# Optimization experiments

Hardware: AMD Instinct MI355X
Metric: run time of the kernel (lower is better)

Reference implementation:

```python
import jax, jax.numpy as jnp
import numpy as np

BN_EPS = 1e-5


def _posit_intervals():
    # Replicates conditions_l1 / conditions_g1 interval tables (128 steps each).
    l1, g1 = [], []
    for e in range(16):
        for j in range(8):
            if j == 0:
                l1.append((0.0, 1.0625 / 2**16, 1.0 / 2**16))
            else:
                lo = (1.0625 + 0.125 * (j - 1)) / 2 ** (16 - e)
                hi = (1.0625 + 0.125 * j) / 2 ** (16 - e)
                l1.append((lo, hi, 0.5 * (lo + hi)))
            lo = (1.0625 + 0.125 * (j - 1)) * 2 ** e
            hi = (1.0625 + 0.125 * j) * 2 ** e
            g1.append((lo, hi, 0.5 * (lo + hi)))  # note: j==8 branch in torch code is dead
    return l1, g1

_L1, _G1 = _posit_intervals()


def posit_quantize(x):
    # Faithful emulation of the 128 sequential torch.where passes.
    ax = jnp.abs(x)          # conditions are fixed from the ORIGINAL tensor
    neg = x < 0
    y = x
    for (lo1, hi1, m1), (log_, hig, mg) in zip(_L1, _G1):
        c1 = jnp.logical_and(ax > lo1, ax < hi1)
        cg = jnp.logical_and(ax > log_, ax < hig)
        v1 = jnp.where(neg, -m1, m1).astype(x.dtype)
        vg = jnp.where(neg, -mg, mg).astype(x.dtype)
        # |y| < 1 gate uses the CURRENT tensor, as in the torch loop
        y = jnp.where(jnp.abs(y) < 1, jnp.where(c1, v1, y), jnp.where(cg, vg, y))
    return y


def conv1x1(x, w, b):
    # x: [N,C,D,H,W], w: [O,C] (kernel_size=1), b: [O]
    return jnp.einsum('ncdhw,oc->nodhw', x, w) + b[None, :, None, None, None]


def batchnorm(x, gamma, beta, mean, var):
    inv = gamma / jnp.sqrt(var + BN_EPS)
    return x * inv[None, :, None, None, None] + (beta - mean * inv)[None, :, None, None, None]


def setup_inputs() -> dict:
    key = jax.random.key(0)
    ks = jax.random.split(key, 12)
    C = 256
    x = jax.random.normal(ks[0], (8, C, 16, 32, 32), dtype=jnp.float32)
    w1 = jax.random.normal(ks[1], (C, C), dtype=jnp.float32) * 0.05
    b1 = jax.random.normal(ks[2], (C,), dtype=jnp.float32) * 0.05
    w2 = jax.random.normal(ks[3], (C, C), dtype=jnp.float32) * 0.05
    b2 = jax.random.normal(ks[4], (C,), dtype=jnp.float32) * 0.05
    g1 = jax.random.uniform(ks[5], (C,)) + 0.5
    be1 = jax.random.normal(ks[6], (C,)) * 0.1
    m1 = jax.random.normal(ks[7], (C,)) * 0.1
    v1 = jax.random.uniform(ks[8], (C,)) + 0.5
    g2 = jax.random.uniform(ks[9], (C,)) + 0.5
    be2 = jax.random.normal(ks[10], (C,)) * 0.1
    m2 = jax.random.normal(ks[11], (C,)) * 0.1
    v2 = jax.random.uniform(jax.random.fold_in(key, 99), (C,)) + 0.5
    return {"x": x, "w1": w1, "b1": b1, "g1": g1, "be1": be1, "m1": m1, "v1": v1,
            "w2": w2, "b2": b2, "g2": g2, "be2": be2, "m2": m2, "v2": v2}


def reference(x, w1, b1, g1, be1, m1, v1, w2, b2, g2, be2, m2, v2):
    residual = x
    out = conv1x1(posit_quantize(x), posit_quantize(w1), b1)
    out = jax.nn.relu(batchnorm(out, g1, be1, m1, v1))
    out = conv1x1(posit_quantize(out), posit_quantize(w2), b2)
    out = batchnorm(out, g2, be2, m2, v2)
    return jax.nn.relu(out + residual)
```

## Files before the change

### kernel.cpp

```cpp
#include <hip/hip_runtime.h>

typedef __attribute__((ext_vector_type(8))) short short8;
typedef __attribute__((ext_vector_type(4))) short s4v;
typedef __attribute__((ext_vector_type(4))) float floatx4;

#define SPOS 16384

__device__ __forceinline__ unsigned short f2bf(float f) {
    unsigned u = __float_as_uint(f);
    u += 0x7fffu + ((u >> 16) & 1u);
    return (unsigned short)(u >> 16);
}

__device__ __forceinline__ float posit_q(float x) {
    unsigned xu  = __float_as_uint(x);
    unsigned sgn = xu & 0x80000000u;
    unsigned au  = xu & 0x7fffffffu;
    unsigned m   = au & 0x007fffffu;
    unsigned r   = (au + 0x00080000u) & 0xfff00000u;
    bool bdry = (m & 0x000fffffu) == 0x00080000u;
    unsigned res;
    if (au >= 0x3f800000u) {
        res = r;
        if (m > 0x00700000u && m < 0x00780000u && au < 0x47700000u)
            res = (au & 0xff800000u) + 0x00800000u;
        if ((bdry && m != 0x00780000u) || au >= 0x47780000u)
            res = au;
    } else {
        res = (m <= 0x00080000u || m >= 0x00780000u || bdry) ? au : r;
        if (au < 0x37880000u) res = au ? 0x37800000u : 0u;
    }
    return __uint_as_float(sgn | res);
}

__global__ __launch_bounds__(256) void prep_kernel(
    const float* __restrict__ w1, const float* __restrict__ w2,
    const float* __restrict__ b1, const float* __restrict__ g1,
    const float* __restrict__ be1, const float* __restrict__ m1,
    const float* __restrict__ v1,
    const float* __restrict__ b2, const float* __restrict__ g2,
    const float* __restrict__ be2, const float* __restrict__ m2,
    const float* __restrict__ v2,
    unsigned short* __restrict__ w1q, unsigned short* __restrict__ w2q,
    float* __restrict__ cst)
{
    int i = blockIdx.x * 256 + threadIdx.x;
    if (i < 65536) {
        w1q[i] = f2bf(posit_q(w1[i]));
        w2q[i] = f2bf(posit_q(w2[i]));
        if (i < 256) {
            float inv1 = g1[i] / sqrtf(v1[i] + 1e-5f);
            cst[i]       = inv1;
            cst[256 + i] = fmaf(b1[i], inv1, be1[i] - m1[i] * inv1);
            float inv2 = g2[i] / sqrtf(v2[i] + 1e-5f);
            cst[512 + i] = inv2;
            cst[768 + i] = fmaf(b2[i], inv2, be2[i] - m2[i] * inv2);
        }
    }
}

__device__ __forceinline__ int qidx(int p, int cb) {
    return p * 256 + ((cb ^ (p & 31)) << 3);
}

__global__ __launch_bounds__(256, 3) void fused_kernel(
    const float* __restrict__ x,
    const unsigned short* __restrict__ w1q,
    const unsigned short* __restrict__ w2q,
    const float* __restrict__ cst,
    float* __restrict__ out)
{
    __shared__ alignas(16) unsigned short q[64 * 256];
    __shared__ alignas(16) float xs[64 * 64];

    const int b  = blockIdx.x;
    const int n  = b >> 8;
    const int s0 = (b & 255) << 6;
    const float* xb = x   + (size_t)n * (256 * SPOS) + s0;
    float*       ob = out + (size_t)n * (256 * SPOS) + s0;

    const int t    = threadIdx.x;
    const int lane = t & 63;
    const int w    = t >> 6;
    const int quad = lane >> 4;
    const int l15  = lane & 15;

    {
        const int g   = t & 15;
        const int ca  = t >> 4;
        for (int qt = 0; qt < 4; ++qt) {
            #pragma unroll
            for (int r = 0; r < 4; ++r) {
                const int cl = r * 16 + ca;
                const float4 v = *(const float4*)&xb[(size_t)(qt * 64 + cl) * SPOS + 4 * g];
                *(float4*)&xs[cl * 64 + 4 * g] = v;
            }
            __syncthreads();
            {
                const int p  = lane;
                const int c0 = w * 16;
                short8 pk0, pk1;
                #pragma unroll
                for (int j = 0; j < 8; ++j) {
                    pk0[j] = (short)f2bf(posit_q(xs[(c0 + j) * 64 + p]));
                    pk1[j] = (short)f2bf(posit_q(xs[(c0 + 8 + j) * 64 + p]));
                }
                const int cb0 = qt * 8 + w * 2;
                *(short8*)&q[qidx(p, cb0)]     = pk0;
                *(short8*)&q[qidx(p, cb0 + 1)] = pk1;
            }
            __syncthreads();
        }
    }

    const int mbase = w * 64;
    floatx4 acc[4][4];
    #pragma unroll
    for (int i = 0; i < 4; ++i)
        #pragma unroll
        for (int jj = 0; jj < 4; ++jj)
            acc[i][jj] = (floatx4)0.0f;

    #pragma unroll
    for (int kk = 0; kk < 256; kk += 32) {
        short8 af[4], bf[4];
        #pragma unroll
        for (int i = 0; i < 4; ++i)
            af[i] = *(const short8*)&w1q[(size_t)(mbase + 16 * i + l15) * 256 + kk + quad * 8];
        #pragma unroll
        for (int jj = 0; jj < 4; ++jj)
            bf[jj] = *(const short8*)&q[qidx(16 * jj + l15, (kk >> 3) + quad)];
        #pragma unroll
        for (int i = 0; i < 4; ++i)
            #pragma unroll
            for (int jj = 0; jj < 4; ++jj)
                acc[i][jj] = __builtin_amdgcn_mfma_f32_16x16x32_bf16(af[i], bf[jj], acc[i][jj], 0, 0, 0);
    }
    __syncthreads();

    {
        const float* sc1 = cst;
        const float* bi1 = cst + 256;
        #pragma unroll
        for (int i = 0; i < 4; ++i) {
            const int m0 = mbase + 16 * i + quad * 4;
            float sc[4], bi[4];
            #pragma unroll
            for (int r = 0; r < 4; ++r) { sc[r] = sc1[m0 + r]; bi[r] = bi1[m0 + r]; }
            #pragma unroll
            for (int jj = 0; jj < 4; ++jj) {
                const int p = 16 * jj + l15;
                s4v h;
                #pragma unroll
                for (int r = 0; r < 4; ++r) {
                    float z = fmaf(acc[i][jj][r], sc[r], bi[r]);
                    z = fmaxf(z, 0.0f);
                    h[r] = (short)f2bf(posit_q(z));
                }
                *(s4v*)&q[qidx(p, m0 >> 3) + (m0 & 7)] = h;
            }
        }
    }
    __syncthreads();

    #pragma unroll
    for (int i = 0; i < 4; ++i)
        #pragma unroll
        for (int jj = 0; jj < 4; ++jj)
            acc[i][jj] = (floatx4)0.0f;

    #pragma unroll
    for (int kk = 0; kk < 256; kk += 32) {
        short8 af[4], bf[4];
        #pragma unroll
        for (int i = 0; i < 4; ++i)
            af[i] = *(const short8*)&w2q[(size_t)(mbase + 16 * i + l15) * 256 + kk + quad * 8];
        #pragma unroll
        for (int jj = 0; jj < 4; ++jj)
            bf[jj] = *(const short8*)&q[qidx(16 * jj + l15, (kk >> 3) + quad)];
        #pragma unroll
        for (int i = 0; i < 4; ++i)
            #pragma unroll
            for (int jj = 0; jj < 4; ++jj)
                acc[i][jj] = __builtin_amdgcn_mfma_f32_16x16x32_bf16(af[i], bf[jj], acc[i][jj], 0, 0, 0);
    }

    {
        const float* sc2 = cst + 512;
        const float* bi2 = cst + 768;
        #pragma unroll
        for (int i = 0; i < 4; ++i) {
            const int m0 = mbase + 16 * i + quad * 4;
            float sc[4], bi[4];
            #pragma unroll
            for (int r = 0; r < 4; ++r) { sc[r] = sc2[m0 + r]; bi[r] = bi2[m0 + r]; }
            #pragma unroll
            for (int jj = 0; jj < 4; ++jj) {
                const int p = 16 * jj + l15;
                #pragma unroll
                for (int r = 0; r < 4; ++r) {
                    const size_t off = (size_t)(m0 + r) * SPOS + p;
                    float v = fmaf(acc[i][jj][r], sc[r], bi[r]);
                    v += xb[off];
                    ob[off] = fmaxf(v, 0.0f);
                }
            }
        }
    }
}

extern "C" void kernel_launch(void* const* d_in, const int* in_sizes, int n_in,
                              void* d_out, int out_size, void* d_ws, size_t ws_size,
                              hipStream_t stream) {
    const float* x   = (const float*)d_in[0];
    const float* w1  = (const float*)d_in[1];
    const float* b1  = (const float*)d_in[2];
    const float* g1  = (const float*)d_in[3];
    const float* be1 = (const float*)d_in[4];
    const float* m1  = (const float*)d_in[5];
    const float* v1  = (const float*)d_in[6];
    const float* w2  = (const float*)d_in[7];
    const float* b2  = (const float*)d_in[8];
    const float* g2  = (const float*)d_in[9];
    const float* be2 = (const float*)d_in[10];
    const float* m2  = (const float*)d_in[11];
    const float* v2  = (const float*)d_in[12];

    unsigned short* w1q = (unsigned short*)d_ws;
    unsigned short* w2q = w1q + 65536;
    float* cst = (float*)(w2q + 65536);

    prep_kernel<<<256, 256, 0, stream>>>(w1, w2, b1, g1, be1, m1, v1,
                                         b2, g2, be2, m2, v2, w1q, w2q, cst);
    fused_kernel<<<2048, 256, 0, stream>>>(x, w1q, w2q, cst, (float*)d_out);
}
```

Baseline: 397.8 us.

## Per-wave x staging with swizzled transpose, drop block barriers, raise occupancy

The input-staging phase changes from four block-wide tiles, each with two __syncthreads, to per-wavefront 8-channel slices in a private 2KB LDS region. Each wave loads, XOR-swizzles, quantizes and packs its own 64 channels, and a single barrier follows. The smaller LDS footprint and launch bounds raised from 3 to 4 are meant to allow more resident blocks per CU. The cost is more sequential load-then-use steps inside each wave and tighter register limits, which could cause spills. Within-wave LDS reuse across iterations relies on the wavefront executing in lockstep.

```diff
diff --git a/kernel.cpp b/kernel.cpp
--- a/kernel.cpp
+++ b/kernel.cpp
@@ -63,7 +63,7 @@
     return p * 256 + ((cb ^ (p & 31)) << 3);
 }
 
-__global__ __launch_bounds__(256, 3) void fused_kernel(
+__global__ __launch_bounds__(256, 4) void fused_kernel(
     const float* __restrict__ x,
     const unsigned short* __restrict__ w1q,
     const unsigned short* __restrict__ w2q,
@@ -71,7 +71,7 @@
     float* __restrict__ out)
 {
     __shared__ alignas(16) unsigned short q[64 * 256];
-    __shared__ alignas(16) float xs[64 * 64];
+    __shared__ alignas(16) float xs[4 * 512];
 
     const int b  = blockIdx.x;
     const int n  = b >> 8;
@@ -86,32 +86,24 @@
     const int l15  = lane & 15;
 
     {
-        const int g   = t & 15;
-        const int ca  = t >> 4;
-        for (int qt = 0; qt < 4; ++qt) {
-            #pragma unroll
-            for (int r = 0; r < 4; ++r) {
-                const int cl = r * 16 + ca;
-                const float4 v = *(const float4*)&xb[(size_t)(qt * 64 + cl) * SPOS + 4 * g];
-                *(float4*)&xs[cl * 64 + 4 * g] = v;
-            }
-            __syncthreads();
-            {
-                const int p  = lane;
-                const int c0 = w * 16;
-                short8 pk0, pk1;
-                #pragma unroll
-                for (int j = 0; j < 8; ++j) {
-                    pk0[j] = (short)f2bf(posit_q(xs[(c0 + j) * 64 + p]));
-                    pk1[j] = (short)f2bf(posit_q(xs[(c0 + 8 + j) * 64 + p]));
-                }
-                const int cb0 = qt * 8 + w * 2;
-                *(short8*)&q[qidx(p, cb0)]     = pk0;
-                *(short8*)&q[qidx(p, cb0 + 1)] = pk1;
-            }
-            __syncthreads();
-        }
-    }
+        const int g  = lane & 15;
+        const int co = lane >> 4;
+        float* xsw = xs + w * 512;
+        const float* src0 = xb + (size_t)(64 * w + co) * SPOS + 4 * g;
+        #pragma unroll
+        for (int r = 0; r < 8; ++r) {
+            const float4 v0 = *(const float4*)(src0 + (size_t)(8 * r) * SPOS);
+            const float4 v1 = *(const float4*)(src0 + (size_t)(8 * r + 4) * SPOS);
+            *(float4*)&xsw[co * 64 + ((4 * g) ^ (4 * co))]             = v0;
+            *(float4*)&xsw[(co + 4) * 64 + ((4 * g) ^ (4 * (co + 4)))] = v1;
+            short8 pk;
+            #pragma unroll
+            for (int c8 = 0; c8 < 8; ++c8)
+                pk[c8] = (short)f2bf(posit_q(xsw[c8 * 64 + (lane ^ (4 * c8))]));
+            *(short8*)&q[qidx(lane, 8 * w + r)] = pk;
+        }
+    }
+    __syncthreads();
 
     const int mbase = w * 64;
     floatx4 acc[4][4];
```

After: 365.7 us. 8.1% less time.
